# Performance work log

Hardware: AMD Instinct MI355X
Metric: run time of the kernel (lower is better)

Reference implementation:

```python
import jax, jax.numpy as jnp
import numpy as np

SEGMENT_LENGTHS = [1024, 2048, 4096]
DILATION_RATES = [1, 2, 4]


def _head_groups(num_heads, num_segments):
    base = num_heads // num_segments
    extra = num_heads % num_segments
    groups = [base] * num_segments
    for i in range(extra):
        groups[-(i + 1)] += 1
    return groups


def _dilated_indices(segment_len, dilation_rate, offset):
    # Mirrors RingDilatedAttentionV2._apply_dilation index construction (static).
    if dilation_rate > 1:
        idx = np.arange(offset, segment_len, dilation_rate)
        repeats = (segment_len + len(idx) - 1) // len(idx)
        idx = np.tile(idx, repeats)[:segment_len] % segment_len
    else:
        idx = np.arange(segment_len)
    return jnp.asarray(idx, dtype=jnp.int32)


def setup_inputs() -> dict:
    key = jax.random.key(0)
    kq, kk, kv = jax.random.split(key, 3)
    b, n, h, d = 1, 4096, 12, 64
    return {
        "query": jax.random.normal(kq, (b, n, h, d), dtype=jnp.float32),
        "key": jax.random.normal(kk, (b, n, h, d), dtype=jnp.float32),
        "value": jax.random.normal(kv, (b, n, h, d), dtype=jnp.float32),
        "is_causal": 1,
    }


def _dilated_attention(query, key, value, is_causal):
    b, n, h, d = query.shape
    groups = _head_groups(h, len(SEGMENT_LENGTHS))
    scale = 1.0 / np.sqrt(d).astype(np.float32)
    outs = []
    head_start = 0
    for i, (seg_len, rate, g) in enumerate(zip(SEGMENT_LENGTHS, DILATION_RATES, groups)):
        if g == 0:
            continue
        sl = min(seg_len, n)
        ns = n // sl  # n chosen divisible by every segment length
        q = query[:, :, head_start:head_start + g, :].reshape(b, ns, sl, g, d)
        k = key[:, :, head_start:head_start + g, :].reshape(b, ns, sl, g, d)
        v = value[:, :, head_start:head_start + g, :].reshape(b, ns, sl, g, d)
        if rate > 1 or i > 0:
            idx = _dilated_indices(sl, rate, i)
            k = k[:, :, idx]
            v = v[:, :, idx]
        # scores: [b, seg, heads, q_pos, k_pos]
        scores = jnp.einsum("bsqhd,bskhd->bshqk", q, k) * scale
        if is_causal:
            causal = jnp.triu(jnp.ones((sl, sl), dtype=bool), k=1)
            scores = jnp.where(causal, jnp.finfo(scores.dtype).min, scores)
        attn = jax.nn.softmax(scores, axis=-1)
        o = jnp.einsum("bshqk,bskhd->bsqhd", attn, v).reshape(b, n, g, d)
        outs.append(o)
        head_start += g
    return jnp.concatenate(outs, axis=2)  # [b, n, h, d]


def reference(query, key, value, is_causal):
    return _dilated_attention(query, key, value, is_causal)
```

## Files before the change

### kernel.cpp

```cpp
#include <hip/hip_runtime.h>
#include <hip/hip_bf16.h>
#include <math.h>

typedef __bf16 bf16x8 __attribute__((ext_vector_type(8)));
typedef float  f32x4  __attribute__((ext_vector_type(4)));
typedef unsigned short ushort_t;

#define LDK 72

#define KG_OFF  0
#define VGT_OFF 6291456
#define LACC_OFF 12582912

__device__ __forceinline__ int gather_pos(int gi, int group) {
    const int lsl = 10 + group;
    const int seg = gi >> lsl;
    const int j   = gi - (seg << lsl);
    return (seg << lsl) + group + ((j & 1023) << group);
}

__global__ __launch_bounds__(256)
void preconvert_kernel(const float* __restrict__ K, const float* __restrict__ V,
                       ushort_t* __restrict__ Kg, ushort_t* __restrict__ VgT)
{
    const int HD = 768;
    int b = blockIdx.x;
    const int tid = threadIdx.x;
    if (b < 768) {
        const int h = b % 12, gi0 = (b / 12) * 64;
        const int group = h >> 2;
        const int gi = gi0 + (tid >> 2);
        const int d0 = (tid & 3) << 4;
        const int pos = gather_pos(gi, group);
        const float* kp = K + (size_t)pos * HD + h * 64 + d0;
        float4 x0 = ((const float4*)kp)[0], x1 = ((const float4*)kp)[1];
        float4 x2 = ((const float4*)kp)[2], x3 = ((const float4*)kp)[3];
        bf16x8 w0, w1;
        w0[0]=(__bf16)x0.x; w0[1]=(__bf16)x0.y; w0[2]=(__bf16)x0.z; w0[3]=(__bf16)x0.w;
        w0[4]=(__bf16)x1.x; w0[5]=(__bf16)x1.y; w0[6]=(__bf16)x1.z; w0[7]=(__bf16)x1.w;
        w1[0]=(__bf16)x2.x; w1[1]=(__bf16)x2.y; w1[2]=(__bf16)x2.z; w1[3]=(__bf16)x2.w;
        w1[4]=(__bf16)x3.x; w1[5]=(__bf16)x3.y; w1[6]=(__bf16)x3.z; w1[7]=(__bf16)x3.w;
        ushort_t* out = Kg + ((size_t)(h * 4096 + gi)) * 64 + d0;
        *(bf16x8*)out = w0;
        *(bf16x8*)(out + 8) = w1;
    } else {
        b -= 768;
        const int h = b % 12, gi0 = (b / 12) * 64;
        const int group = h >> 2;
        __shared__ __align__(16) __bf16 Ts[64 * LDK];
        const int gil = tid >> 2;
        const int d0 = (tid & 3) << 4;
        const int pos = gather_pos(gi0 + gil, group);
        const float* vp = V + (size_t)pos * HD + h * 64 + d0;
        float4 x0 = ((const float4*)vp)[0], x1 = ((const float4*)vp)[1];
        float4 x2 = ((const float4*)vp)[2], x3 = ((const float4*)vp)[3];
        bf16x8 w0, w1;
        w0[0]=(__bf16)x0.x; w0[1]=(__bf16)x0.y; w0[2]=(__bf16)x0.z; w0[3]=(__bf16)x0.w;
        w0[4]=(__bf16)x1.x; w0[5]=(__bf16)x1.y; w0[6]=(__bf16)x1.z; w0[7]=(__bf16)x1.w;
        w1[0]=(__bf16)x2.x; w1[1]=(__bf16)x2.y; w1[2]=(__bf16)x2.z; w1[3]=(__bf16)x2.w;
        w1[4]=(__bf16)x3.x; w1[5]=(__bf16)x3.y; w1[6]=(__bf16)x3.z; w1[7]=(__bf16)x3.w;
        *(bf16x8*)&Ts[gil * LDK + d0]     = w0;
        *(bf16x8*)&Ts[gil * LDK + d0 + 8] = w1;
        __syncthreads();
        const int d = tid >> 2, c = tid & 3;
        bf16x8 o0, o1;
        #pragma unroll
        for (int i = 0; i < 8; ++i) {
            o0[i] = Ts[(c * 16 + i) * LDK + d];
            o1[i] = Ts[(c * 16 + 8 + i) * LDK + d];
        }
        ushort_t* out = VgT + ((size_t)(h * 64 + d)) * 4096 + gi0 + c * 16;
        *(bf16x8*)out = o0;
        *(bf16x8*)(out + 8) = o1;
    }
}

__global__ __launch_bounds__(256)
void dilated_attn_kernel(const float* __restrict__ Q,
                         const ushort_t* __restrict__ Kg,
                         const ushort_t* __restrict__ VgT,
                         const int* __restrict__ is_causal_p,
                         float* __restrict__ Out,
                         float* __restrict__ l_acc)
{
    const int HD = 768;
    const int bx  = blockIdx.x;
    const int qt  = 63 - (bx / 48);
    const int rem = bx % 48;
    const int h   = rem % 12;
    const int c   = rem / 12;
    const int group = h >> 2;
    const int sl    = 1024 << group;
    const int causal = (*is_causal_p) != 0;

    const int q0 = qt << 6;
    const int qb = q0 & (sl - 1);
    const int seg_start = q0 - qb;
    const int diag_kt = qb >> 6;
    const int nkt = causal ? (diag_kt + 1) : (sl >> 6);
    const int kt0 = c << 4;
    if (kt0 >= nkt) return;
    const int kend = min(kt0 + 16, nkt);
    const int nch  = (nkt + 15) >> 4;

    const int tid  = threadIdx.x;
    const int wave = tid >> 6;
    const int lane = tid & 63;
    const int l15  = lane & 15;
    const int quad = lane >> 4;

    __shared__ __align__(16) __bf16 Ks[2][64 * LDK];
    __shared__ __align__(16) __bf16 Vs[2][64 * LDK];
    __shared__ __align__(16) __bf16 Ps[4][16 * LDK];

    const int srow = tid >> 3;
    const int scol = (tid & 7) << 3;
    const ushort_t* kg_head = Kg + (size_t)h * 4096 * 64;
    const ushort_t* vt_head = VgT + (size_t)h * 64 * 4096;

    const int qrow = q0 + wave * 16 + l15;
    const float* qptr = Q + (size_t)qrow * HD + h * 64;
    bf16x8 a0, a1;
    {
        const float s = 0.125f * 1.4426950408889634f;
        float4 x0 = ((const float4*)(qptr + quad * 8))[0];
        float4 x1 = ((const float4*)(qptr + quad * 8))[1];
        float4 y0 = ((const float4*)(qptr + 32 + quad * 8))[0];
        float4 y1 = ((const float4*)(qptr + 32 + quad * 8))[1];
        a0[0]=(__bf16)(x0.x*s); a0[1]=(__bf16)(x0.y*s); a0[2]=(__bf16)(x0.z*s); a0[3]=(__bf16)(x0.w*s);
        a0[4]=(__bf16)(x1.x*s); a0[5]=(__bf16)(x1.y*s); a0[6]=(__bf16)(x1.z*s); a0[7]=(__bf16)(x1.w*s);
        a1[0]=(__bf16)(y0.x*s); a1[1]=(__bf16)(y0.y*s); a1[2]=(__bf16)(y0.z*s); a1[3]=(__bf16)(y0.w*s);
        a1[4]=(__bf16)(y1.x*s); a1[5]=(__bf16)(y1.y*s); a1[6]=(__bf16)(y1.z*s); a1[7]=(__bf16)(y1.w*s);
    }

    f32x4 o[4];
    #pragma unroll
    for (int t = 0; t < 4; ++t) o[t] = (f32x4){0.f, 0.f, 0.f, 0.f};
    float l_r[4] = {0.f, 0.f, 0.f, 0.f};

    bf16x8 kr0, kr1, vr0, vr1;
    auto load_tile = [&](int kt) {
        const ushort_t* kb = kg_head + (size_t)(seg_start + (kt << 6)) * 64;
        kr0 = *(const bf16x8*)(kb + srow * 64 + scol);
        kr1 = *(const bf16x8*)(kb + (srow + 32) * 64 + scol);
        const ushort_t* vb = vt_head + seg_start + (kt << 6);
        vr0 = *(const bf16x8*)(vb + (size_t)srow * 4096 + scol);
        vr1 = *(const bf16x8*)(vb + (size_t)(srow + 32) * 4096 + scol);
    };
    auto store_tile = [&](int buf) {
        *(bf16x8*)&Ks[buf][srow * LDK + scol]        = kr0;
        *(bf16x8*)&Ks[buf][(srow + 32) * LDK + scol] = kr1;
        *(bf16x8*)&Vs[buf][srow * LDK + scol]        = vr0;
        *(bf16x8*)&Vs[buf][(srow + 32) * LDK + scol] = vr1;
    };

    load_tile(kt0);
    store_tile(0);
    __syncthreads();

    for (int kt = kt0; kt < kend; ++kt) {
        const int cur = (kt - kt0) & 1;
        const bool more = (kt + 1 < kend);
        if (more) load_tile(kt + 1);

        f32x4 sacc[4];
        #pragma unroll
        for (int t = 0; t < 4; ++t) {
            bf16x8 b0 = *(const bf16x8*)&Ks[cur][(t * 16 + l15) * LDK + quad * 8];
            bf16x8 b1 = *(const bf16x8*)&Ks[cur][(t * 16 + l15) * LDK + 32 + quad * 8];
            f32x4 cc = (f32x4){0.f, 0.f, 0.f, 0.f};
            cc = __builtin_amdgcn_mfma_f32_16x16x32_bf16(a0, b0, cc, 0, 0, 0);
            cc = __builtin_amdgcn_mfma_f32_16x16x32_bf16(a1, b1, cc, 0, 0, 0);
            sacc[t] = cc;
        }

        const bool isdiag = causal && (kt == diag_kt);
        #pragma unroll
        for (int t = 0; t < 4; ++t) {
            const int col = t * 16 + l15;
            #pragma unroll
            for (int r = 0; r < 4; ++r) {
                const int row = wave * 16 + quad * 4 + r;
                float p = exp2f(sacc[t][r]);
                if (isdiag && col > row) p = 0.f;
                l_r[r] += p;
                Ps[wave][(quad * 4 + r) * LDK + t * 16 + l15] = (__bf16)p;
            }
        }

        bf16x8 p0 = *(const bf16x8*)&Ps[wave][l15 * LDK + quad * 8];
        bf16x8 p1 = *(const bf16x8*)&Ps[wave][l15 * LDK + 32 + quad * 8];
        #pragma unroll
        for (int t = 0; t < 4; ++t) {
            bf16x8 bv0 = *(const bf16x8*)&Vs[cur][(t * 16 + l15) * LDK + quad * 8];
            bf16x8 bv1 = *(const bf16x8*)&Vs[cur][(t * 16 + l15) * LDK + 32 + quad * 8];
            o[t] = __builtin_amdgcn_mfma_f32_16x16x32_bf16(p0, bv0, o[t], 0, 0, 0);
            o[t] = __builtin_amdgcn_mfma_f32_16x16x32_bf16(p1, bv1, o[t], 0, 0, 0);
        }

        if (more) store_tile(cur ^ 1);
        __syncthreads();
    }

    #pragma unroll
    for (int off = 1; off < 16; off <<= 1) {
        #pragma unroll
        for (int r = 0; r < 4; ++r)
            l_r[r] += __shfl_xor(l_r[r], off, 64);
    }
    if (nch == 1) {
        #pragma unroll
        for (int r = 0; r < 4; ++r) {
            const float inv = 1.0f / l_r[r];
            const int row = q0 + wave * 16 + quad * 4 + r;
            #pragma unroll
            for (int t = 0; t < 4; ++t)
                Out[(size_t)row * HD + h * 64 + t * 16 + l15] = o[t][r] * inv;
        }
    } else {
        #pragma unroll
        for (int r = 0; r < 4; ++r) {
            const int row = q0 + wave * 16 + quad * 4 + r;
            if (l15 == 0) atomicAdd(&l_acc[row * 12 + h], l_r[r]);
            #pragma unroll
            for (int t = 0; t < 4; ++t)
                atomicAdd(&Out[(size_t)row * HD + h * 64 + t * 16 + l15], o[t][r]);
        }
    }
}

__global__ __launch_bounds__(256)
void finalize_kernel(float* __restrict__ Out, const float* __restrict__ l_acc,
                     const int* __restrict__ is_causal_p)
{
    const int causal = (*is_causal_p) != 0;
    const int idx = blockIdx.x * 256 + threadIdx.x;
    const int rh = idx >> 4;
    const int d4 = idx & 15;
    const int h = rh % 12;
    const int row = rh / 12;
    const int group = h >> 2;
    const int ntf = 16 << group;
    const int qt = row >> 6;
    const int nkt = causal ? ((qt & (ntf - 1)) + 1) : ntf;
    if (nkt <= 16) return;
    const float inv = 1.0f / l_acc[rh];
    float4* p = (float4*)Out + (size_t)rh * 16 + d4;
    float4 v = *p;
    v.x *= inv; v.y *= inv; v.z *= inv; v.w *= inv;
    *p = v;
}

extern "C" void kernel_launch(void* const* d_in, const int* in_sizes, int n_in,
                              void* d_out, int out_size, void* d_ws, size_t ws_size,
                              hipStream_t stream) {
    (void)in_sizes; (void)n_in; (void)out_size; (void)ws_size;
    const float* Q = (const float*)d_in[0];
    const float* K = (const float*)d_in[1];
    const float* V = (const float*)d_in[2];
    const int* isc = (const int*)d_in[3];
    float* Out = (float*)d_out;
    ushort_t* Kg   = (ushort_t*)((char*)d_ws + KG_OFF);
    ushort_t* VgT  = (ushort_t*)((char*)d_ws + VGT_OFF);
    float*    lacc = (float*)((char*)d_ws + LACC_OFF);

    hipMemsetAsync(Out, 0, (size_t)4096 * 12 * 64 * 4, stream);
    hipMemsetAsync(lacc, 0, (size_t)4096 * 12 * 4, stream);
    preconvert_kernel<<<1536, 256, 0, stream>>>(K, V, Kg, VgT);
    dilated_attn_kernel<<<3072, 256, 0, stream>>>(Q, Kg, VgT, isc, Out, lacc);
    finalize_kernel<<<3072, 256, 0, stream>>>(Out, lacc, isc);
}
```

Measured before the change: 149.3 us.

## Stage K/V tiles via direct global-to-LDS loads with XOR-swizzled layout

Replaces the register-staged K/V tile loads (global to VGPR, then ds_write) with global_load_lds 16-byte direct-to-LDS transfers. The padded LDK=72 layout is swapped for an unpadded 64-wide layout with XOR swizzling on K, V and P to avoid bank conflicts. s_setprio hints are added around the MFMA sections. The aim is to cut VGPR pressure and LDS write instructions, at the cost of relying on a correct swizzle mapping and on async LDS-load ordering through the existing barrier.

```diff
diff --git a/kernel.cpp b/kernel.cpp
--- a/kernel.cpp
+++ b/kernel.cpp
@@ -17,6 +17,12 @@
     const int seg = gi >> lsl;
     const int j   = gi - (seg << lsl);
     return (seg << lsl) + group + ((j & 1023) << group);
+}
+
+__device__ __forceinline__ void gld_lds16(const ushort_t* g, __bf16* l) {
+    __builtin_amdgcn_global_load_lds(
+        (const __attribute__((address_space(1))) void*)g,
+        (__attribute__((address_space(3))) void*)l, 16, 0, 0);
 }
 
 __global__ __launch_bounds__(256)
@@ -109,14 +115,30 @@
     const int l15  = lane & 15;
     const int quad = lane >> 4;
 
-    __shared__ __align__(16) __bf16 Ks[2][64 * LDK];
-    __shared__ __align__(16) __bf16 Vs[2][64 * LDK];
-    __shared__ __align__(16) __bf16 Ps[4][16 * LDK];
-
-    const int srow = tid >> 3;
-    const int scol = (tid & 7) << 3;
+    __shared__ __align__(16) __bf16 Ks[2][64 * 64];
+    __shared__ __align__(16) __bf16 Vs[2][64 * 64];
+    __shared__ __align__(16) __bf16 Ps[4][16 * 64];
+
     const ushort_t* kg_head = Kg + (size_t)h * 4096 * 64;
     const ushort_t* vt_head = VgT + (size_t)h * 64 * 4096;
+
+    const int bx16  = ((lane & 7) ^ (lane >> 3)) << 3;
+    const int krow0 = wave * 16 + (lane >> 3);
+    const int koff0 = krow0 * 64 + bx16;
+    const int koff1 = koff0 + 8 * 64;
+    const size_t voff0 = (size_t)krow0 * 4096 + bx16;
+    const size_t voff1 = voff0 + (size_t)8 * 4096;
+
+    auto stage = [&](int kt, int buf) {
+        const ushort_t* kb = kg_head + ((size_t)(seg_start + (kt << 6)) << 6);
+        const ushort_t* vb = vt_head + seg_start + (kt << 6);
+        __bf16* kl = &Ks[buf][wave * 1024];
+        __bf16* vl = &Vs[buf][wave * 1024];
+        gld_lds16(kb + koff0, kl);
+        gld_lds16(kb + koff1, kl + 512);
+        gld_lds16(vb + voff0, vl);
+        gld_lds16(vb + voff1, vl + 512);
+    };
 
     const int qrow = q0 + wave * 16 + l15;
     const float* qptr = Q + (size_t)qrow * HD + h * 64;
@@ -138,67 +160,59 @@
     for (int t = 0; t < 4; ++t) o[t] = (f32x4){0.f, 0.f, 0.f, 0.f};
     float l_r[4] = {0.f, 0.f, 0.f, 0.f};
 
-    bf16x8 kr0, kr1, vr0, vr1;
-    auto load_tile = [&](int kt) {
-        const ushort_t* kb = kg_head + (size_t)(seg_start + (kt << 6)) * 64;
-        kr0 = *(const bf16x8*)(kb + srow * 64 + scol);
-        kr1 = *(const bf16x8*)(kb + (srow + 32) * 64 + scol);
-        const ushort_t* vb = vt_head + seg_start + (kt << 6);
-        vr0 = *(const bf16x8*)(vb + (size_t)srow * 4096 + scol);
-        vr1 = *(const bf16x8*)(vb + (size_t)(srow + 32) * 4096 + scol);
-    };
-    auto store_tile = [&](int buf) {
-        *(bf16x8*)&Ks[buf][srow * LDK + scol]        = kr0;
-        *(bf16x8*)&Ks[buf][(srow + 32) * LDK + scol] = kr1;
-        *(bf16x8*)&Vs[buf][srow * LDK + scol]        = vr0;
-        *(bf16x8*)&Vs[buf][(srow + 32) * LDK + scol] = vr1;
-    };
-
-    load_tile(kt0);
-    store_tile(0);
+    stage(kt0, 0);
     __syncthreads();
 
     for (int kt = kt0; kt < kend; ++kt) {
         const int cur = (kt - kt0) & 1;
-        const bool more = (kt + 1 < kend);
-        if (more) load_tile(kt + 1);
+        if (kt + 1 < kend) stage(kt + 1, cur ^ 1);
 
         f32x4 sacc[4];
+        __builtin_amdgcn_s_setprio(1);
         #pragma unroll
         for (int t = 0; t < 4; ++t) {
-            bf16x8 b0 = *(const bf16x8*)&Ks[cur][(t * 16 + l15) * LDK + quad * 8];
-            bf16x8 b1 = *(const bf16x8*)&Ks[cur][(t * 16 + l15) * LDK + 32 + quad * 8];
+            const int krow = t * 16 + l15;
+            const int xk = (krow & 7) << 3;
+            bf16x8 b0 = *(const bf16x8*)&Ks[cur][krow * 64 + ((quad << 3) ^ xk)];
+            bf16x8 b1 = *(const bf16x8*)&Ks[cur][krow * 64 + (((quad + 4) << 3) ^ xk)];
             f32x4 cc = (f32x4){0.f, 0.f, 0.f, 0.f};
             cc = __builtin_amdgcn_mfma_f32_16x16x32_bf16(a0, b0, cc, 0, 0, 0);
             cc = __builtin_amdgcn_mfma_f32_16x16x32_bf16(a1, b1, cc, 0, 0, 0);
             sacc[t] = cc;
         }
+        __builtin_amdgcn_s_setprio(0);
 
         const bool isdiag = causal && (kt == diag_kt);
         #pragma unroll
         for (int t = 0; t < 4; ++t) {
             const int col = t * 16 + l15;
+            const int cb  = t * 2 + (l15 >> 3);
             #pragma unroll
             for (int r = 0; r < 4; ++r) {
-                const int row = wave * 16 + quad * 4 + r;
+                const int prow = quad * 4 + r;
+                const int row = wave * 16 + prow;
                 float p = exp2f(sacc[t][r]);
                 if (isdiag && col > row) p = 0.f;
                 l_r[r] += p;
-                Ps[wave][(quad * 4 + r) * LDK + t * 16 + l15] = (__bf16)p;
+                Ps[wave][prow * 64 + ((cb ^ (prow & 7)) << 3) + (l15 & 7)] = (__bf16)p;
             }
         }
 
-        bf16x8 p0 = *(const bf16x8*)&Ps[wave][l15 * LDK + quad * 8];
-        bf16x8 p1 = *(const bf16x8*)&Ps[wave][l15 * LDK + 32 + quad * 8];
+        const int xp = (l15 & 7) << 3;
+        bf16x8 p0 = *(const bf16x8*)&Ps[wave][l15 * 64 + ((quad << 3) ^ xp)];
+        bf16x8 p1 = *(const bf16x8*)&Ps[wave][l15 * 64 + (((quad + 4) << 3) ^ xp)];
+        __builtin_amdgcn_s_setprio(1);
         #pragma unroll
         for (int t = 0; t < 4; ++t) {
-            bf16x8 bv0 = *(const bf16x8*)&Vs[cur][(t * 16 + l15) * LDK + quad * 8];
-            bf16x8 bv1 = *(const bf16x8*)&Vs[cur][(t * 16 + l15) * LDK + 32 + quad * 8];
+            const int vrow = t * 16 + l15;
+            const int xv = (vrow & 7) << 3;
+            bf16x8 bv0 = *(const bf16x8*)&Vs[cur][vrow * 64 + ((quad << 3) ^ xv)];
+            bf16x8 bv1 = *(const bf16x8*)&Vs[cur][vrow * 64 + (((quad + 4) << 3) ^ xv)];
             o[t] = __builtin_amdgcn_mfma_f32_16x16x32_bf16(p0, bv0, o[t], 0, 0, 0);
             o[t] = __builtin_amdgcn_mfma_f32_16x16x32_bf16(p1, bv1, o[t], 0, 0, 0);
         }
-
-        if (more) store_tile(cur ^ 1);
+        __builtin_amdgcn_s_setprio(0);
+
         __syncthreads();
     }
 
```

After: 155.3 us. +4.0%, slower.
